# Kernel optimization log

Measured on AMD Instinct MI355X. Metric: run time of the kernel, lower is better.

## Reference

```python
import jax, jax.numpy as jnp
import numpy as np


def setup_inputs() -> dict:
    key = jax.random.key(0)
    N, M, D = 2048, 16, 128
    x = jax.random.normal(key, (N, M, D), dtype=jnp.float32)
    # usage normalizes embeddings before the loss (F.normalize(p=2, dim=-1))
    x = x / jnp.linalg.norm(x, axis=-1, keepdims=True)
    w = jnp.float32(10.0)   # learnable scale, init per GE2ELoss.__init__
    b = jnpp if False else jnp.float32(-5.0)  # learnable bias
    return {"x": x, "w": w, "b": b}


def reference(x, w, b):
    N, M, D = x.shape
    # full centroid per speaker (N, D)
    centroids = jnp.mean(x, axis=1)
    # bulk of cos_sim is a plain GEMM: (N, M, D) x (N, D) -> (N, M, N)
    sim = jnp.einsum('nmd,kd->nmk', x, centroids)
    # leave-one-out centroid for the row's own speaker: (M*c_n - x_nm)/(M-1)
    excl = (M * centroids[:, None, :] - x) / (M - 1)      # (N, M, D)
    diag = jnp.sum(x * excl, axis=-1)                     # (N, M)
    n_idx = jnp.arange(N)[:, None]                        # (N, 1)
    m_idx = jnp.arange(M)[None, :]                        # (1, M)
    # overwrite self-speaker column with leave-one-out similarity
    sim = sim.at[n_idx, m_idx, n_idx].set(diag)
    logits = w * sim + b                                  # (N, M, N)
    logp = jax.nn.log_softmax(logits, axis=-1)
    # cross-entropy with target = own speaker id, mean over all N*M rows
    loss = -jnp.mean(logp[n_idx, m_idx, n_idx])
    return loss
```

## Files before the change

kernel.cpp:

```cpp
#include <hip/hip_runtime.h>

typedef __bf16 bf16_t;
typedef __bf16 bf16x8 __attribute__((ext_vector_type(8)));
typedef float f32x4 __attribute__((ext_vector_type(4)));

#define L2E 1.44269504088896340736f
#define LN2 0.69314718055994530942f

#define N 2048
#define M 16
#define D 128
#define NM (N * M)
#define NCG 16

__global__ __launch_bounds__(128) void prep_kernel(
    const float* __restrict__ x, bf16_t* __restrict__ xb,
    bf16_t* __restrict__ cb, float* __restrict__ dnn,
    float* __restrict__ diag, float* __restrict__ out) {
  int n = blockIdx.x, t = threadIdx.x;
  if (n == 0 && t == 0) *out = 0.f;
  __shared__ float sc[D];
  const float* xr = x + (size_t)n * (M * D);
  float xv[M];
  float c = 0.f;
#pragma unroll
  for (int m = 0; m < M; ++m) {
    xv[m] = xr[m * D + t];
    c += xv[m];
  }
  c *= (1.f / M);
  sc[t] = c;
  cb[n * D + t] = (bf16_t)c;
#pragma unroll
  for (int m = 0; m < M; ++m)
    xb[(size_t)n * (M * D) + m * D + t] = (bf16_t)xv[m];
  __syncthreads();
  int m = t >> 3, j = t & 7;
  float p = 0.f, q = 0.f;
#pragma unroll
  for (int i = 0; i < 16; ++i) {
    int d = j * 16 + i;
    float xd = xr[m * D + d];
    float cd = sc[d];
    p += xd * cd;
    q += xd * xd;
  }
  p += __shfl_xor(p, 1); p += __shfl_xor(p, 2); p += __shfl_xor(p, 4);
  q += __shfl_xor(q, 1); q += __shfl_xor(q, 2); q += __shfl_xor(q, 4);
  if (j == 0) {
    dnn[n * M + m] = p;
    diag[n * M + m] = (16.f * p - q) * (1.f / 15.f);
  }
}

#define TSTR 136

__global__ __launch_bounds__(256) void main_kernel(
    const bf16_t* __restrict__ xb, const bf16_t* __restrict__ cb,
    const float* __restrict__ wp, const float* __restrict__ bp,
    float* __restrict__ rowsum_p) {
  __shared__ bf16_t tile[128 * TSTR];
  int t = threadIdx.x;
  int rg = blockIdx.x >> 4;
  int cg = blockIdx.x & 15;
  int R0 = rg * 256, C0 = cg * 128;

#pragma unroll
  for (int i = 0; i < 8; ++i) {
    int col = i * 16 + (t >> 4);
    int k = (t & 15) * 8;
    uint4 v = *(const uint4*)(cb + (size_t)(C0 + col) * D + k);
    *(uint4*)(&tile[col * TSTR + k]) = v;
  }

  int w = t >> 6, lane = t & 63;
  int la = lane & 15, lb = lane >> 4;
  int rowbase = R0 + w * 64;

  bf16x8 a[4][4];
#pragma unroll
  for (int rt = 0; rt < 4; ++rt)
#pragma unroll
    for (int kc = 0; kc < 4; ++kc)
      a[rt][kc] = *(const bf16x8*)(xb + (size_t)(rowbase + rt * 16 + la) * D +
                                   kc * 32 + lb * 8);
  __syncthreads();

  float wv = wp[0], bv = bp[0];
  float wsc = wv * L2E, bsc = bv * L2E;
  float sums[4][4];
#pragma unroll
  for (int rt = 0; rt < 4; ++rt)
#pragma unroll
    for (int r = 0; r < 4; ++r) sums[rt][r] = 0.f;

#pragma unroll
  for (int cs = 0; cs < 8; ++cs) {
    bf16x8 bfr[4];
    const bf16_t* b0 = &tile[(cs * 16 + la) * TSTR + lb * 8];
#pragma unroll
    for (int kc = 0; kc < 4; ++kc) bfr[kc] = *(const bf16x8*)(b0 + kc * 32);
#pragma unroll
    for (int rt = 0; rt < 4; ++rt) {
      f32x4 acc = {0.f, 0.f, 0.f, 0.f};
#pragma unroll
      for (int kc = 0; kc < 4; ++kc)
        acc = __builtin_amdgcn_mfma_f32_16x16x32_bf16(a[rt][kc], bfr[kc], acc,
                                                      0, 0, 0);
#pragma unroll
      for (int r = 0; r < 4; ++r)
        sums[rt][r] += __builtin_amdgcn_exp2f(acc[r] * wsc + bsc);
    }
  }

  float* rp = rowsum_p + (size_t)cg * NM;
#pragma unroll
  for (int rt = 0; rt < 4; ++rt)
#pragma unroll
    for (int r = 0; r < 4; ++r) {
      float v = sums[rt][r];
      v += __shfl_xor(v, 1); v += __shfl_xor(v, 2);
      v += __shfl_xor(v, 4); v += __shfl_xor(v, 8);
      if (la == 0)
        rp[rowbase + rt * 16 + lb * 4 + r] = v;
    }
}

__global__ __launch_bounds__(256) void finish_kernel(
    const float* __restrict__ rowsum_p, const float* __restrict__ dnn,
    const float* __restrict__ diag, const float* __restrict__ wp,
    const float* __restrict__ bp, float* __restrict__ out) {
  int i = blockIdx.x * 256 + threadIdx.x;
  float wv = wp[0], bv = bp[0];
  float S0 = 0.f;
#pragma unroll
  for (int k = 0; k < NCG; ++k) S0 += rowsum_p[(size_t)k * NM + i];
  float tnn = (wv * dnn[i] + bv) * L2E;
  float sself = wv * diag[i] + bv;
  float S = S0 - __builtin_amdgcn_exp2f(tnn) +
            __builtin_amdgcn_exp2f(sself * L2E);
  float lr = __builtin_amdgcn_logf(S) * LN2 - sself;
#pragma unroll
  for (int off = 1; off < 64; off <<= 1) lr += __shfl_xor(lr, off);
  __shared__ float red[4];
  int lane = threadIdx.x & 63, wid = threadIdx.x >> 6;
  if (lane == 0) red[wid] = lr;
  __syncthreads();
  if (threadIdx.x == 0)
    atomicAdd(out, (red[0] + red[1] + red[2] + red[3]) * (1.f / NM));
}

extern "C" void kernel_launch(void* const* d_in, const int* in_sizes, int n_in,
                              void* d_out, int out_size, void* d_ws,
                              size_t ws_size, hipStream_t stream) {
  (void)in_sizes; (void)n_in; (void)out_size; (void)ws_size;
  const float* x = (const float*)d_in[0];
  const float* wp = (const float*)d_in[1];
  const float* bp = (const float*)d_in[2];
  float* out = (float*)d_out;

  char* ws = (char*)d_ws;
  bf16_t* xb = (bf16_t*)ws;
  bf16_t* cb = (bf16_t*)(ws + 8388608);
  float* dnn = (float*)(ws + 8912896);
  float* diag = (float*)(ws + 9043968);
  float* rowsum_p = (float*)(ws + 9175040);

  prep_kernel<<<N, 128, 0, stream>>>(x, xb, cb, dnn, diag, out);
  main_kernel<<<2048, 256, 0, stream>>>(xb, cb, wp, bp, rowsum_p);
  finish_kernel<<<NM / 256, 256, 0, stream>>>(rowsum_p, dnn, diag, wp, bp,
                                              out);
}
```

Measured before the change: 107.3 us.

## Switch GEMM operands to FP8 with scaled MFMA and mask self column in-kernel

```diff
diff --git a/kernel.cpp b/kernel.cpp
--- a/kernel.cpp
+++ b/kernel.cpp
@@ -1,8 +1,7 @@
 #include <hip/hip_runtime.h>
 
-typedef __bf16 bf16_t;
-typedef __bf16 bf16x8 __attribute__((ext_vector_type(8)));
 typedef float f32x4 __attribute__((ext_vector_type(4)));
+typedef int i32x8 __attribute__((ext_vector_type(8)));
 
 #define L2E 1.44269504088896340736f
 #define LN2 0.69314718055994530942f
@@ -13,10 +12,15 @@
 #define NM (N * M)
 #define NCG 16
 
+__device__ __forceinline__ unsigned char f32_to_f8(float v) {
+  return (unsigned char)(__builtin_amdgcn_cvt_pk_fp8_f32(v, v, 0, false) &
+                         0xff);
+}
+
 __global__ __launch_bounds__(128) void prep_kernel(
-    const float* __restrict__ x, bf16_t* __restrict__ xb,
-    bf16_t* __restrict__ cb, float* __restrict__ dnn,
-    float* __restrict__ diag, float* __restrict__ out) {
+    const float* __restrict__ x, unsigned char* __restrict__ xb8,
+    unsigned char* __restrict__ cb8, float* __restrict__ diag,
+    float* __restrict__ out) {
   int n = blockIdx.x, t = threadIdx.x;
   if (n == 0 && t == 0) *out = 0.f;
   __shared__ float sc[D];
@@ -30,10 +34,10 @@
   }
   c *= (1.f / M);
   sc[t] = c;
-  cb[n * D + t] = (bf16_t)c;
+  cb8[n * D + t] = f32_to_f8(c);
 #pragma unroll
   for (int m = 0; m < M; ++m)
-    xb[(size_t)n * (M * D) + m * D + t] = (bf16_t)xv[m];
+    xb8[(size_t)(n * M + m) * D + t] = f32_to_f8(xv[m]);
   __syncthreads();
   int m = t >> 3, j = t & 7;
   float p = 0.f, q = 0.f;
@@ -47,47 +51,50 @@
   }
   p += __shfl_xor(p, 1); p += __shfl_xor(p, 2); p += __shfl_xor(p, 4);
   q += __shfl_xor(q, 1); q += __shfl_xor(q, 2); q += __shfl_xor(q, 4);
-  if (j == 0) {
-    dnn[n * M + m] = p;
-    diag[n * M + m] = (16.f * p - q) * (1.f / 15.f);
-  }
+  if (j == 0) diag[n * M + m] = (16.f * p - q) * (1.f / 15.f);
 }
 
-#define TSTR 136
+#define TS 144
 
 __global__ __launch_bounds__(256) void main_kernel(
-    const bf16_t* __restrict__ xb, const bf16_t* __restrict__ cb,
-    const float* __restrict__ wp, const float* __restrict__ bp,
-    float* __restrict__ rowsum_p) {
-  __shared__ bf16_t tile[128 * TSTR];
+    const unsigned char* __restrict__ xb8,
+    const unsigned char* __restrict__ cb8, const float* __restrict__ wp,
+    const float* __restrict__ bp, float* __restrict__ rowsum_p) {
+  __shared__ uint4 tileq[128 * TS / 16];
+  unsigned char* tile = (unsigned char*)tileq;
   int t = threadIdx.x;
   int rg = blockIdx.x >> 4;
   int cg = blockIdx.x & 15;
   int R0 = rg * 256, C0 = cg * 128;
 
 #pragma unroll
-  for (int i = 0; i < 8; ++i) {
-    int col = i * 16 + (t >> 4);
-    int k = (t & 15) * 8;
-    uint4 v = *(const uint4*)(cb + (size_t)(C0 + col) * D + k);
-    *(uint4*)(&tile[col * TSTR + k]) = v;
+  for (int i = 0; i < 4; ++i) {
+    int col = i * 32 + (t >> 3);
+    int k = (t & 7) * 16;
+    *(uint4*)(tile + col * TS + k) =
+        *(const uint4*)(cb8 + (size_t)(C0 + col) * D + k);
   }
 
   int w = t >> 6, lane = t & 63;
   int la = lane & 15, lb = lane >> 4;
   int rowbase = R0 + w * 64;
 
-  bf16x8 a[4][4];
+  i32x8 a[4];
 #pragma unroll
-  for (int rt = 0; rt < 4; ++rt)
-#pragma unroll
-    for (int kc = 0; kc < 4; ++kc)
-      a[rt][kc] = *(const bf16x8*)(xb + (size_t)(rowbase + rt * 16 + la) * D +
-                                   kc * 32 + lb * 8);
+  for (int rt = 0; rt < 4; ++rt) {
+    const unsigned char* ap =
+        xb8 + (size_t)(rowbase + rt * 16 + la) * D + lb * 32;
+    uint4 a0 = *(const uint4*)(ap);
+    uint4 a1 = *(const uint4*)(ap + 16);
+    a[rt] = (i32x8){(int)a0.x, (int)a0.y, (int)a0.z, (int)a0.w,
+                    (int)a1.x, (int)a1.y, (int)a1.z, (int)a1.w};
+  }
   __syncthreads();
 
   float wv = wp[0], bv = bp[0];
   float wsc = wv * L2E, bsc = bv * L2E;
+  int selfcs = (cg == (rg >> 3)) ? (rg & 7) : -1;
+
   float sums[4][4];
 #pragma unroll
   for (int rt = 0; rt < 4; ++rt)
@@ -96,20 +103,22 @@
 
 #pragma unroll
   for (int cs = 0; cs < 8; ++cs) {
-    bf16x8 bfr[4];
-    const bf16_t* b0 = &tile[(cs * 16 + la) * TSTR + lb * 8];
-#pragma unroll
-    for (int kc = 0; kc < 4; ++kc) bfr[kc] = *(const bf16x8*)(b0 + kc * 32);
+    const unsigned char* bp8 = tile + (cs * 16 + la) * TS + lb * 32;
+    uint4 b0 = *(const uint4*)(bp8);
+    uint4 b1 = *(const uint4*)(bp8 + 16);
+    i32x8 bf = (i32x8){(int)b0.x, (int)b0.y, (int)b0.z, (int)b0.w,
+                       (int)b1.x, (int)b1.y, (int)b1.z, (int)b1.w};
 #pragma unroll
     for (int rt = 0; rt < 4; ++rt) {
       f32x4 acc = {0.f, 0.f, 0.f, 0.f};
+      acc = __builtin_amdgcn_mfma_scale_f32_16x16x128_f8f6f4(
+          a[rt], bf, acc, 0, 0, 0, 0x7f7f7f7f, 0, 0x7f7f7f7f);
+      bool notself = !(cs == selfcs && la == ((w << 2) | rt));
 #pragma unroll
-      for (int kc = 0; kc < 4; ++kc)
-        acc = __builtin_amdgcn_mfma_f32_16x16x32_bf16(a[rt][kc], bfr[kc], acc,
-                                                      0, 0, 0);
-#pragma unroll
-      for (int r = 0; r < 4; ++r)
-        sums[rt][r] += __builtin_amdgcn_exp2f(acc[r] * wsc + bsc);
+      for (int r = 0; r < 4; ++r) {
+        float e = __builtin_amdgcn_exp2f(acc[r] * wsc + bsc);
+        sums[rt][r] += notself ? e : 0.f;
+      }
     }
   }
 
@@ -127,18 +136,16 @@
 }
 
 __global__ __launch_bounds__(256) void finish_kernel(
-    const float* __restrict__ rowsum_p, const float* __restrict__ dnn,
-    const float* __restrict__ diag, const float* __restrict__ wp,
-    const float* __restrict__ bp, float* __restrict__ out) {
+    const float* __restrict__ rowsum_p, const float* __restrict__ diag,
+    const float* __restrict__ wp, const float* __restrict__ bp,
+    float* __restrict__ out) {
   int i = blockIdx.x * 256 + threadIdx.x;
   float wv = wp[0], bv = bp[0];
   float S0 = 0.f;
 #pragma unroll
   for (int k = 0; k < NCG; ++k) S0 += rowsum_p[(size_t)k * NM + i];
-  float tnn = (wv * dnn[i] + bv) * L2E;
   float sself = wv * diag[i] + bv;
-  float S = S0 - __builtin_amdgcn_exp2f(tnn) +
-            __builtin_amdgcn_exp2f(sself * L2E);
+  float S = S0 + __builtin_amdgcn_exp2f(sself * L2E);
   float lr = __builtin_amdgcn_logf(S) * LN2 - sself;
 #pragma unroll
   for (int off = 1; off < 64; off <<= 1) lr += __shfl_xor(lr, off);
@@ -160,14 +167,12 @@
   float* out = (float*)d_out;
 
   char* ws = (char*)d_ws;
-  bf16_t* xb = (bf16_t*)ws;
-  bf16_t* cb = (bf16_t*)(ws + 8388608);
-  float* dnn = (float*)(ws + 8912896);
-  float* diag = (float*)(ws + 9043968);
-  float* rowsum_p = (float*)(ws + 9175040);
+  unsigned char* xb8 = (unsigned char*)ws;
+  unsigned char* cb8 = (unsigned char*)(ws + 4194304);
+  float* diag = (float*)(ws + 4456448);
+  float* rowsum_p = (float*)(ws + 4587520);
 
-  prep_kernel<<<N, 128, 0, stream>>>(x, xb, cb, dnn, diag, out);
-  main_kernel<<<2048, 256, 0, stream>>>(xb, cb, wp, bp, rowsum_p);
-  finish_kernel<<<NM / 256, 256, 0, stream>>>(rowsum_p, dnn, diag, wp, bp,
-                                              out);
+  prep_kernel<<<N, 128, 0, stream>>>(x, xb8, cb8, diag, out);
+  main_kernel<<<2048, 256, 0, stream>>>(xb8, cb8, wp, bp, rowsum_p);
+  finish_kernel<<<NM / 256, 256, 0, stream>>>(rowsum_p, diag, wp, bp, out);
 }
```

New measurement: 96.88 us. 1.11x faster.
